# Kernel optimization log

Hardware: AMD Instinct MI355X
Metric: run time of the kernel (lower is better)

The kernel has to match this reference:

```python
import jax, jax.numpy as jnp
import numpy as np

N_EMBD = 1024
HEAD_SIZE = 64
B, T = 16, 2048


def setup_inputs() -> dict:
    key = jax.random.key(0)
    ks = jax.random.split(key, 7)
    s = 1.0 / np.sqrt(N_EMBD)
    return {
        "x": jax.random.normal(ks[0], (B, T, N_EMBD), dtype=jnp.float32),
        "Wq": jax.random.uniform(ks[1], (N_EMBD, HEAD_SIZE), jnp.float32, -s, s),
        "bq": jax.random.uniform(ks[2], (HEAD_SIZE,), jnp.float32, -s, s),
        "Wk": jax.random.uniform(ks[3], (N_EMBD, HEAD_SIZE), jnp.float32, -s, s),
        "bk": jax.random.uniform(ks[4], (HEAD_SIZE,), jnp.float32, -s, s),
        "Wv": jax.random.uniform(ks[5], (N_EMBD, HEAD_SIZE), jnp.float32, -s, s),
        "bv": jax.random.uniform(ks[6], (HEAD_SIZE,), jnp.float32, -s, s),
    }


def reference(x, Wq, bq, Wk, bk, Wv, bv):
    # x: [B, T, C]
    q = x @ Wq + bq          # [B, T, H]
    k = x @ Wk + bk          # [B, T, H]
    v = x @ Wv + bv          # [B, T, H]
    scale = k.shape[-1] ** -0.5
    wei = jnp.einsum("bth,bsh->bts", q, k) * scale  # [B, T, T]
    Tn = x.shape[1]
    causal = jnp.tril(jnp.ones((Tn, Tn), dtype=bool))
    wei = jnp.where(causal, wei, -jnp.inf)
    wei = jax.nn.softmax(wei, axis=-1)
    # dropout is identity in eval mode
    return jnp.einsum("bts,bsh->bth", wei, v)  # [B, T, H]
```

## Files before the change

### kernel.cpp

```cpp
#include <hip/hip_runtime.h>
#include <math.h>

#define BB 16
#define TT 2048
#define CC 1024
#define HH 64
#define MTOT (BB*TT)

typedef _Float16 f16;
typedef _Float16 f16x8 __attribute__((ext_vector_type(8)));
typedef float f32x4 __attribute__((ext_vector_type(4)));

#define WT_OFF 0
#define Q_OFF  196608
#define K_OFF  (Q_OFF + (size_t)MTOT*HH)
#define VT_OFF (K_OFF + (size_t)MTOT*HH)

__device__ __forceinline__ void async16(const void* g, void* l) {
    __builtin_amdgcn_global_load_lds(
        (const __attribute__((address_space(1))) unsigned int*)g,
        (__attribute__((address_space(3))) unsigned int*)l, 16, 0, 0);
}

__device__ __forceinline__ f16x8 cvt8(float4 u, float4 v) {
    f16x8 r;
    r[0] = (f16)u.x; r[1] = (f16)u.y; r[2] = (f16)u.z; r[3] = (f16)u.w;
    r[4] = (f16)v.x; r[5] = (f16)v.y; r[6] = (f16)v.z; r[7] = (f16)v.w;
    return r;
}

__global__ __launch_bounds__(256) void prep_kernel(
    const float* __restrict__ Wq, const float* __restrict__ Wk,
    const float* __restrict__ Wv, f16* __restrict__ ws)
{
    int e = blockIdx.x * 256 + threadIdx.x;
    int ng = e >> 10, k = e & 1023;
    int which = ng >> 6, n = ng & 63;
    const float* W = (which == 0) ? Wq : (which == 1) ? Wk : Wv;
    ws[WT_OFF + e] = (f16)W[k * HH + n];
}

__global__ __launch_bounds__(256, 2) void qkv_kernel(
    const float* __restrict__ x,
    const float* __restrict__ bq, const float* __restrict__ bk,
    const float* __restrict__ bv, f16* __restrict__ ws)
{
    __shared__ __align__(16) float Xs[64 * 64];
    __shared__ __align__(16) f16   Ws[192 * 64];
    __shared__ __align__(16) f16   Vt[64][72];

    const f16* wt = ws + WT_OFF;
    const int tid  = threadIdx.x;
    const int lane = tid & 63, w = tid >> 6;
    const int c = lane & 15, g = lane >> 4;
    const int m0 = blockIdx.x * 64;

    f32x4 acc[4][3];
    #pragma unroll
    for (int mt = 0; mt < 4; ++mt)
        #pragma unroll
        for (int j = 0; j < 3; ++j) acc[mt][j] = (f32x4){0.f, 0.f, 0.f, 0.f};

    for (int k0 = 0; k0 < CC; k0 += 64) {
        __syncthreads();
        #pragma unroll
        for (int i = 0; i < 4; ++i) {
            int G0 = (w * 4 + i) * 64;
            int G = G0 + lane;
            int r = G >> 4, q = G & 15;
            async16(x + (size_t)(m0 + r) * CC + k0 + ((q ^ (r & 15)) << 2),
                    Xs + G0 * 4);
        }
        #pragma unroll
        for (int i = 0; i < 6; ++i) {
            int G0 = (w * 6 + i) * 64;
            int G = G0 + lane;
            int r = G >> 3, q = G & 7;
            async16(wt + (size_t)r * CC + k0 + ((q ^ (r & 7)) << 3),
                    Ws + G0 * 8);
        }
        __syncthreads();

        #pragma unroll
        for (int kk = 0; kk < 2; ++kk) {
            f16x8 bfr[3];
            #pragma unroll
            for (int j = 0; j < 3; ++j) {
                int r = (3 * w + j) * 16 + c;
                int p = (kk * 4 + g) ^ (c & 7);
                bfr[j] = *(const f16x8*)(Ws + r * 64 + p * 8);
            }
            #pragma unroll
            for (int mt = 0; mt < 4; ++mt) {
                int r = mt * 16 + c;
                int q = kk * 8 + 2 * g;
                float4 f0 = *(const float4*)(Xs + r * 64 + (q ^ c) * 4);
                float4 f1 = *(const float4*)(Xs + r * 64 + ((q + 1) ^ c) * 4);
                f16x8 a = cvt8(f0, f1);
                #pragma unroll
                for (int j = 0; j < 3; ++j)
                    acc[mt][j] = __builtin_amdgcn_mfma_f32_16x16x32_f16(
                        a, bfr[j], acc[mt][j], 0, 0, 0);
            }
        }
    }

    #pragma unroll
    for (int j = 0; j < 3; ++j) {
        int nt = 3 * w + j;
        int plane = nt >> 2;
        int h = (nt & 3) * 16 + c;
        if (plane == 0) {
            float bias = bq[h];
            #pragma unroll
            for (int mt = 0; mt < 4; ++mt)
                #pragma unroll
                for (int r = 0; r < 4; ++r) {
                    int m = m0 + mt * 16 + 4 * g + r;
                    ws[Q_OFF + (size_t)m * HH + h] =
                        (f16)((acc[mt][j][r] + bias) * 0.125f);
                }
        } else if (plane == 1) {
            float bias = bk[h];
            #pragma unroll
            for (int mt = 0; mt < 4; ++mt)
                #pragma unroll
                for (int r = 0; r < 4; ++r) {
                    int m = m0 + mt * 16 + 4 * g + r;
                    ws[K_OFF + (size_t)m * HH + h] = (f16)(acc[mt][j][r] + bias);
                }
        } else {
            float bias = bv[h];
            #pragma unroll
            for (int mt = 0; mt < 4; ++mt)
                #pragma unroll
                for (int r = 0; r < 4; ++r)
                    Vt[h][mt * 16 + 4 * g + r] = (f16)(acc[mt][j][r] + bias);
        }
    }
    __syncthreads();
    {
        int h = tid >> 2, seg = tid & 3;
        f16* dst = ws + VT_OFF + (size_t)h * MTOT + m0 + seg * 16;
        *(f16x8*)dst       = *(f16x8*)&Vt[h][seg * 16];
        *(f16x8*)(dst + 8) = *(f16x8*)&Vt[h][seg * 16 + 8];
    }
}

__global__ __launch_bounds__(256, 2) void attn_kernel(
    const f16* __restrict__ ws, float* __restrict__ out)
{
    const f16* qp = ws + Q_OFF;
    const f16* kp = ws + K_OFF;
    const f16* vt = ws + VT_OFF;

    __shared__ __align__(16) f16 Qs[64 * 64];
    __shared__ __align__(16) f16 Ks[64 * 64];
    __shared__ __align__(16) f16 Vs[64 * 64];
    __shared__ __align__(16) f16 Ps[4][16][72];

    const int tid  = threadIdx.x;
    const int lane = tid & 63, w = tid >> 6;
    const int c = lane & 15, g = lane >> 4;

    const int id = blockIdx.x;
    const int r8 = id & 7, j = id >> 3;
    const int half = j >> 5, qr = j & 31;
    const int b  = 2 * r8 + half;
    const int qi = half ? (31 - qr) : qr;
    const int q0 = qi * 64;
    const size_t rowbase = (size_t)b * TT;

    #pragma unroll
    for (int i = 0; i < 2; ++i) {
        int G0 = (w * 2 + i) * 64;
        int G = G0 + lane;
        int r = G >> 3, q = G & 7;
        async16(qp + (rowbase + q0 + r) * HH + ((q ^ (r & 7)) << 3),
                Qs + G0 * 8);
    }

    f32x4 o[5];
    #pragma unroll
    for (int nt = 0; nt < 5; ++nt) o[nt] = (f32x4){0.f, 0.f, 0.f, 0.f};

    f16x8 onesf;
    #pragma unroll
    for (int i = 0; i < 8; ++i) onesf[i] = (c == 0) ? (f16)1.0f : (f16)0.0f;

    for (int st = 0; st <= qi; ++st) {
        const int s0 = st * 64;
        __syncthreads();
        #pragma unroll
        for (int i = 0; i < 2; ++i) {
            int G0 = (w * 2 + i) * 64;
            int G = G0 + lane;
            int r = G >> 3, q = G & 7;
            int sw = (q ^ (r & 7)) << 3;
            async16(kp + (rowbase + s0 + r) * HH + sw, Ks + G0 * 8);
            async16(vt + (size_t)r * MTOT + rowbase + s0 + sw, Vs + G0 * 8);
        }
        __syncthreads();

        f16x8 aq[2];
        {
            int r = w * 16 + c;
            aq[0] = *(const f16x8*)(Qs + r * 64 + ((g)     ^ (c & 7)) * 8);
            aq[1] = *(const f16x8*)(Qs + r * 64 + ((4 + g) ^ (c & 7)) * 8);
        }

        f32x4 s[4];
        #pragma unroll
        for (int nt = 0; nt < 4; ++nt) {
            s[nt] = (f32x4){0.f, 0.f, 0.f, 0.f};
            int r = nt * 16 + c;
            f16x8 b0 = *(const f16x8*)(Ks + r * 64 + ((g)     ^ (c & 7)) * 8);
            f16x8 b1 = *(const f16x8*)(Ks + r * 64 + ((4 + g) ^ (c & 7)) * 8);
            s[nt] = __builtin_amdgcn_mfma_f32_16x16x32_f16(aq[0], b0, s[nt], 0, 0, 0);
            s[nt] = __builtin_amdgcn_mfma_f32_16x16x32_f16(aq[1], b1, s[nt], 0, 0, 0);
        }

        if (st == qi) {
            #pragma unroll
            for (int nt = 0; nt < 4; ++nt)
                #pragma unroll
                for (int rr = 0; rr < 4; ++rr)
                    if (nt * 16 + c > w * 16 + 4 * g + rr) s[nt][rr] = -INFINITY;
        }

        #pragma unroll
        for (int nt = 0; nt < 4; ++nt)
            #pragma unroll
            for (int rr = 0; rr < 4; ++rr)
                Ps[w][4 * g + rr][nt * 16 + c] = (f16)__expf(s[nt][rr]);
        f16x8 pa0 = *(f16x8*)&Ps[w][c][g * 8];
        f16x8 pa1 = *(f16x8*)&Ps[w][c][32 + g * 8];

        #pragma unroll
        for (int nt = 0; nt < 4; ++nt) {
            int r = nt * 16 + c;
            f16x8 v0 = *(const f16x8*)(Vs + r * 64 + ((g)     ^ (c & 7)) * 8);
            f16x8 v1 = *(const f16x8*)(Vs + r * 64 + ((4 + g) ^ (c & 7)) * 8);
            o[nt] = __builtin_amdgcn_mfma_f32_16x16x32_f16(pa0, v0, o[nt], 0, 0, 0);
            o[nt] = __builtin_amdgcn_mfma_f32_16x16x32_f16(pa1, v1, o[nt], 0, 0, 0);
        }
        o[4] = __builtin_amdgcn_mfma_f32_16x16x32_f16(pa0, onesf, o[4], 0, 0, 0);
        o[4] = __builtin_amdgcn_mfma_f32_16x16x32_f16(pa1, onesf, o[4], 0, 0, 0);
    }

    #pragma unroll
    for (int rr = 0; rr < 4; ++rr) {
        float lv = __shfl(o[4][rr], lane & 48);
        float inv = 1.0f / lv;
        int mrow = q0 + w * 16 + 4 * g + rr;
        #pragma unroll
        for (int nt = 0; nt < 4; ++nt)
            out[(rowbase + mrow) * HH + nt * 16 + c] = o[nt][rr] * inv;
    }
}

extern "C" void kernel_launch(void* const* d_in, const int* in_sizes, int n_in,
                              void* d_out, int out_size, void* d_ws, size_t ws_size,
                              hipStream_t stream) {
    const float* x  = (const float*)d_in[0];
    const float* Wq = (const float*)d_in[1];
    const float* bq = (const float*)d_in[2];
    const float* Wk = (const float*)d_in[3];
    const float* bk = (const float*)d_in[4];
    const float* Wv = (const float*)d_in[5];
    const float* bv = (const float*)d_in[6];
    f16*   ws  = (f16*)d_ws;
    float* out = (float*)d_out;

    prep_kernel<<<768, 256, 0, stream>>>(Wq, Wk, Wv, ws);
    qkv_kernel<<<MTOT / 64, 256, 0, stream>>>(x, bq, bk, bv, ws);
    dim3 g2(512);
    attn_kernel<<<g2, 256, 0, stream>>>(ws, out);
}
```

Measured before the change: 242.9 us.

## Register-prefetch QKV GEMM, LDS-transpose weight prep, exp2 softmax, register Q

The QKV projection no longer stages tiles in LDS. Each wave loads x and the f16 weights straight from global memory into double-buffered registers, using a smaller 32-row tile and launch bounds raised to three blocks. Weight prep now transposes through shared memory with coalesced vector loads and stores instead of strided scalar reads. In attention, the log2(e) factor is folded into the Q scale so exp2 replaces expf, and Q fragments are held in registers rather than LDS. The trade-off is higher register pressure and the loss of data reuse through LDS in the GEMM.

```diff
diff --git a/kernel.cpp b/kernel.cpp
--- a/kernel.cpp
+++ b/kernel.cpp
@@ -33,78 +33,102 @@
     const float* __restrict__ Wq, const float* __restrict__ Wk,
     const float* __restrict__ Wv, f16* __restrict__ ws)
 {
-    int e = blockIdx.x * 256 + threadIdx.x;
-    int ng = e >> 10, k = e & 1023;
-    int which = ng >> 6, n = ng & 63;
+    __shared__ f16 Ls[64][72];
+    const int which = blockIdx.x >> 4, k0 = (blockIdx.x & 15) * 64;
     const float* W = (which == 0) ? Wq : (which == 1) ? Wk : Wv;
-    ws[WT_OFF + e] = (f16)W[k * HH + n];
-}
-
-__global__ __launch_bounds__(256, 2) void qkv_kernel(
+    const int t = threadIdx.x;
+    const int kr = t >> 2, cb = t & 3;
+    #pragma unroll
+    for (int i = 0; i < 4; ++i) {
+        float4 v = *(const float4*)(W + (size_t)(k0 + kr) * HH + cb * 16 + i * 4);
+        Ls[kr][cb * 16 + i * 4 + 0] = (f16)v.x;
+        Ls[kr][cb * 16 + i * 4 + 1] = (f16)v.y;
+        Ls[kr][cb * 16 + i * 4 + 2] = (f16)v.z;
+        Ls[kr][cb * 16 + i * 4 + 3] = (f16)v.w;
+    }
+    __syncthreads();
+    const int n = t >> 2, kc = (t & 3) * 16;
+    f16x8 o0, o1;
+    #pragma unroll
+    for (int i = 0; i < 8; ++i) o0[i] = Ls[kc + i][n];
+    #pragma unroll
+    for (int i = 0; i < 8; ++i) o1[i] = Ls[kc + 8 + i][n];
+    f16* dst = ws + WT_OFF + (size_t)(which * 64 + n) * CC + k0 + kc;
+    *(f16x8*)dst = o0;
+    *(f16x8*)(dst + 8) = o1;
+}
+
+__global__ __launch_bounds__(256, 3) void qkv_kernel(
     const float* __restrict__ x,
     const float* __restrict__ bq, const float* __restrict__ bk,
     const float* __restrict__ bv, f16* __restrict__ ws)
 {
-    __shared__ __align__(16) float Xs[64 * 64];
-    __shared__ __align__(16) f16   Ws[192 * 64];
-    __shared__ __align__(16) f16   Vt[64][72];
+    __shared__ __align__(16) f16 Vt[64][36];
 
     const f16* wt = ws + WT_OFF;
     const int tid  = threadIdx.x;
     const int lane = tid & 63, w = tid >> 6;
     const int c = lane & 15, g = lane >> 4;
-    const int m0 = blockIdx.x * 64;
-
-    f32x4 acc[4][3];
-    #pragma unroll
-    for (int mt = 0; mt < 4; ++mt)
+    const int m0 = blockIdx.x * 32;
+
+    f32x4 acc[2][3];
+    #pragma unroll
+    for (int mt = 0; mt < 2; ++mt)
         #pragma unroll
         for (int j = 0; j < 3; ++j) acc[mt][j] = (f32x4){0.f, 0.f, 0.f, 0.f};
 
-    for (int k0 = 0; k0 < CC; k0 += 64) {
-        __syncthreads();
-        #pragma unroll
-        for (int i = 0; i < 4; ++i) {
-            int G0 = (w * 4 + i) * 64;
-            int G = G0 + lane;
-            int r = G >> 4, q = G & 15;
-            async16(x + (size_t)(m0 + r) * CC + k0 + ((q ^ (r & 15)) << 2),
-                    Xs + G0 * 4);
-        }
-        #pragma unroll
-        for (int i = 0; i < 6; ++i) {
-            int G0 = (w * 6 + i) * 64;
-            int G = G0 + lane;
-            int r = G >> 3, q = G & 7;
-            async16(wt + (size_t)r * CC + k0 + ((q ^ (r & 7)) << 3),
-                    Ws + G0 * 8);
-        }
-        __syncthreads();
-
-        #pragma unroll
-        for (int kk = 0; kk < 2; ++kk) {
-            f16x8 bfr[3];
-            #pragma unroll
-            for (int j = 0; j < 3; ++j) {
-                int r = (3 * w + j) * 16 + c;
-                int p = (kk * 4 + g) ^ (c & 7);
-                bfr[j] = *(const f16x8*)(Ws + r * 64 + p * 8);
-            }
-            #pragma unroll
-            for (int mt = 0; mt < 4; ++mt) {
-                int r = mt * 16 + c;
-                int q = kk * 8 + 2 * g;
-                float4 f0 = *(const float4*)(Xs + r * 64 + (q ^ c) * 4);
-                float4 f1 = *(const float4*)(Xs + r * 64 + ((q + 1) ^ c) * 4);
-                f16x8 a = cvt8(f0, f1);
-                #pragma unroll
-                for (int j = 0; j < 3; ++j)
-                    acc[mt][j] = __builtin_amdgcn_mfma_f32_16x16x32_f16(
-                        a, bfr[j], acc[mt][j], 0, 0, 0);
-            }
-        }
-    }
-
+    float4 xv[2][8];
+    f16x8  wv[2][6];
+
+    const float* xr0 = x + (size_t)(m0 + c) * CC + 8 * g;
+    const float* xr1 = x + (size_t)(m0 + 16 + c) * CC + 8 * g;
+    const f16* wr[3];
+    #pragma unroll
+    for (int j = 0; j < 3; ++j)
+        wr[j] = wt + (size_t)((3 * w + j) * 16 + c) * CC + 8 * g;
+
+    #define LOADSTEP(buf, k0)                                             \
+        do {                                                              \
+            _Pragma("unroll")                                             \
+            for (int kk = 0; kk < 2; ++kk) {                              \
+                xv[buf][0 * 4 + kk * 2 + 0] = *(const float4*)(xr0 + (k0) + kk * 32);     \
+                xv[buf][0 * 4 + kk * 2 + 1] = *(const float4*)(xr0 + (k0) + kk * 32 + 4); \
+                xv[buf][1 * 4 + kk * 2 + 0] = *(const float4*)(xr1 + (k0) + kk * 32);     \
+                xv[buf][1 * 4 + kk * 2 + 1] = *(const float4*)(xr1 + (k0) + kk * 32 + 4); \
+            }                                                             \
+            _Pragma("unroll")                                             \
+            for (int j = 0; j < 3; ++j)                                   \
+                _Pragma("unroll")                                         \
+                for (int kk = 0; kk < 2; ++kk)                            \
+                    wv[buf][j * 2 + kk] = *(const f16x8*)(wr[j] + (k0) + kk * 32); \
+        } while (0)
+
+    #define COMPSTEP(buf)                                                 \
+        do {                                                              \
+            _Pragma("unroll")                                             \
+            for (int kk = 0; kk < 2; ++kk) {                              \
+                f16x8 a0 = cvt8(xv[buf][kk * 2], xv[buf][kk * 2 + 1]);    \
+                f16x8 a1 = cvt8(xv[buf][4 + kk * 2], xv[buf][4 + kk * 2 + 1]); \
+                _Pragma("unroll")                                         \
+                for (int j = 0; j < 3; ++j) {                             \
+                    acc[0][j] = __builtin_amdgcn_mfma_f32_16x16x32_f16(   \
+                        a0, wv[buf][j * 2 + kk], acc[0][j], 0, 0, 0);     \
+                    acc[1][j] = __builtin_amdgcn_mfma_f32_16x16x32_f16(   \
+                        a1, wv[buf][j * 2 + kk], acc[1][j], 0, 0, 0);     \
+                }                                                         \
+            }                                                             \
+        } while (0)
+
+    LOADSTEP(0, 0);
+    #pragma unroll
+    for (int t = 0; t < 16; ++t) {
+        if (t < 15) LOADSTEP((t + 1) & 1, (t + 1) * 64);
+        COMPSTEP(t & 1);
+    }
+    #undef LOADSTEP
+    #undef COMPSTEP
+
+    const float QSCALE = 0.125f * 1.44269504089f;
     #pragma unroll
     for (int j = 0; j < 3; ++j) {
         int nt = 3 * w + j;
@@ -113,17 +137,17 @@
         if (plane == 0) {
             float bias = bq[h];
             #pragma unroll
-            for (int mt = 0; mt < 4; ++mt)
+            for (int mt = 0; mt < 2; ++mt)
                 #pragma unroll
                 for (int r = 0; r < 4; ++r) {
                     int m = m0 + mt * 16 + 4 * g + r;
                     ws[Q_OFF + (size_t)m * HH + h] =
-                        (f16)((acc[mt][j][r] + bias) * 0.125f);
+                        (f16)((acc[mt][j][r] + bias) * QSCALE);
                 }
         } else if (plane == 1) {
             float bias = bk[h];
             #pragma unroll
-            for (int mt = 0; mt < 4; ++mt)
+            for (int mt = 0; mt < 2; ++mt)
                 #pragma unroll
                 for (int r = 0; r < 4; ++r) {
                     int m = m0 + mt * 16 + 4 * g + r;
@@ -132,15 +156,15 @@
         } else {
             float bias = bv[h];
             #pragma unroll
-            for (int mt = 0; mt < 4; ++mt)
+            for (int mt = 0; mt < 2; ++mt)
                 #pragma unroll
                 for (int r = 0; r < 4; ++r)
                     Vt[h][mt * 16 + 4 * g + r] = (f16)(acc[mt][j][r] + bias);
         }
     }
     __syncthreads();
-    {
-        int h = tid >> 2, seg = tid & 3;
+    if (tid < 128) {
+        int h = tid >> 1, seg = tid & 1;
         f16* dst = ws + VT_OFF + (size_t)h * MTOT + m0 + seg * 16;
         *(f16x8*)dst       = *(f16x8*)&Vt[h][seg * 16];
         *(f16x8*)(dst + 8) = *(f16x8*)&Vt[h][seg * 16 + 8];
@@ -154,7 +178,6 @@
     const f16* kp = ws + K_OFF;
     const f16* vt = ws + VT_OFF;
 
-    __shared__ __align__(16) f16 Qs[64 * 64];
     __shared__ __align__(16) f16 Ks[64 * 64];
     __shared__ __align__(16) f16 Vs[64 * 64];
     __shared__ __align__(16) f16 Ps[4][16][72];
@@ -171,14 +194,9 @@
     const int q0 = qi * 64;
     const size_t rowbase = (size_t)b * TT;
 
-    #pragma unroll
-    for (int i = 0; i < 2; ++i) {
-        int G0 = (w * 2 + i) * 64;
-        int G = G0 + lane;
-        int r = G >> 3, q = G & 7;
-        async16(qp + (rowbase + q0 + r) * HH + ((q ^ (r & 7)) << 3),
-                Qs + G0 * 8);
-    }
+    const f16* qrow = qp + (rowbase + q0 + w * 16 + c) * HH;
+    const f16x8 aq0 = *(const f16x8*)(qrow + 8 * g);
+    const f16x8 aq1 = *(const f16x8*)(qrow + 32 + 8 * g);
 
     f32x4 o[5];
     #pragma unroll
@@ -202,22 +220,15 @@
         }
         __syncthreads();
 
-        f16x8 aq[2];
-        {
-            int r = w * 16 + c;
-            aq[0] = *(const f16x8*)(Qs + r * 64 + ((g)     ^ (c & 7)) * 8);
-            aq[1] = *(const f16x8*)(Qs + r * 64 + ((4 + g) ^ (c & 7)) * 8);
-        }
-
         f32x4 s[4];
         #pragma unroll
         for (int nt = 0; nt < 4; ++nt) {
             s[nt] = (f32x4){0.f, 0.f, 0.f, 0.f};
             int r = nt * 16 + c;
-            f16x8 b0 = *(const f16x8*)(Ks + r * 64 + ((g)     ^ (c & 7)) * 8);
-            f16x8 b1 = *(const f16x8*)(Ks + r * 64 + ((4 + g) ^ (c & 7)) * 8);
-            s[nt] = __builtin_amdgcn_mfma_f32_16x16x32_f16(aq[0], b0, s[nt], 0, 0, 0);
-            s[nt] = __builtin_amdgcn_mfma_f32_16x16x32_f16(aq[1], b1, s[nt], 0, 0, 0);
+            f16x8 b0 = *(const f16x8*)(Ks + r * 64 + ((g       ^ (c & 7)) << 3));
+            f16x8 b1 = *(const f16x8*)(Ks + r * 64 + (((4 + g) ^ (c & 7)) << 3));
+            s[nt] = __builtin_amdgcn_mfma_f32_16x16x32_f16(aq0, b0, s[nt], 0, 0, 0);
+            s[nt] = __builtin_amdgcn_mfma_f32_16x16x32_f16(aq1, b1, s[nt], 0, 0, 0);
         }
 
         if (st == qi) {
@@ -232,15 +243,15 @@
         for (int nt = 0; nt < 4; ++nt)
             #pragma unroll
             for (int rr = 0; rr < 4; ++rr)
-                Ps[w][4 * g + rr][nt * 16 + c] = (f16)__expf(s[nt][rr]);
+                Ps[w][4 * g + rr][nt * 16 + c] = (f16)__builtin_exp2f(s[nt][rr]);
         f16x8 pa0 = *(f16x8*)&Ps[w][c][g * 8];
         f16x8 pa1 = *(f16x8*)&Ps[w][c][32 + g * 8];
 
         #pragma unroll
         for (int nt = 0; nt < 4; ++nt) {
             int r = nt * 16 + c;
-            f16x8 v0 = *(const f16x8*)(Vs + r * 64 + ((g)     ^ (c & 7)) * 8);
-            f16x8 v1 = *(const f16x8*)(Vs + r * 64 + ((4 + g) ^ (c & 7)) * 8);
+            f16x8 v0 = *(const f16x8*)(Vs + r * 64 + ((g       ^ (c & 7)) << 3));
+            f16x8 v1 = *(const f16x8*)(Vs + r * 64 + (((4 + g) ^ (c & 7)) << 3));
             o[nt] = __builtin_amdgcn_mfma_f32_16x16x32_f16(pa0, v0, o[nt], 0, 0, 0);
             o[nt] = __builtin_amdgcn_mfma_f32_16x16x32_f16(pa1, v1, o[nt], 0, 0, 0);
         }
@@ -272,8 +283,7 @@
     f16*   ws  = (f16*)d_ws;
     float* out = (float*)d_out;
 
-    prep_kernel<<<768, 256, 0, stream>>>(Wq, Wk, Wv, ws);
-    qkv_kernel<<<MTOT / 64, 256, 0, stream>>>(x, bq, bk, bv, ws);
-    dim3 g2(512);
-    attn_kernel<<<g2, 256, 0, stream>>>(ws, out);
-}
+    prep_kernel<<<48, 256, 0, stream>>>(Wq, Wk, Wv, ws);
+    qkv_kernel<<<MTOT / 32, 256, 0, stream>>>(x, bq, bk, bv, ws);
+    attn_kernel<<<512, 256, 0, stream>>>(ws, out);
+}
```

Measured after the change: 308.4 us. 1.27x slower.
